# Kernel tuning notes

Hardware: AMD Instinct MI355X
Metric: run time of the kernel (lower is better)

## Reference

```python
import jax, jax.numpy as jnp
import numpy as np

B, S, C = 64, 1024, 512
EPS = 1e-5

def setup_inputs() -> dict:
    key = jax.random.key(0)
    k1, k2, k3 = jax.random.split(key, 3)
    x = jax.random.normal(k1, (B, S, C), dtype=jnp.float32)
    # LayerNorm affine over normalized_shape=[S, C]
    ln_w = jnp.ones((S, C), dtype=jnp.float32)
    ln_b = jnp.zeros((S, C), dtype=jnp.float32)
    # Linear(seq_len, seq_len): torch init U(-1/sqrt(S), 1/sqrt(S))
    bound = 1.0 / np.sqrt(S)
    lin_w = jax.random.uniform(k2, (S, S), jnp.float32, -bound, bound)
    lin_b = jax.random.uniform(k3, (S,), jnp.float32, -bound, bound)
    return {"x": x, "ln_w": ln_w, "ln_b": ln_b, "lin_w": lin_w, "lin_b": lin_b}

def reference(x, ln_w, ln_b, lin_w, lin_b):
    # LayerNorm over last two dims [S, C]
    mu = jnp.mean(x, axis=(1, 2), keepdims=True)
    var = jnp.mean(jnp.square(x - mu), axis=(1, 2), keepdims=True)
    h = (x - mu) * jax.lax.rsqrt(var + EPS) * ln_w + ln_b
    # permute -> [B, C, S], linear over S, relu, permute back, residual
    # fused as einsum over the seq axis directly (no explicit transpose)
    y = jnp.einsum('bsc,ts->btc', h, lin_w) + lin_b[None, :, None]
    y = jax.nn.relu(y)
    return x + y
```

## Files before the change

kernel.cpp:

```cpp
#include <hip/hip_runtime.h>
#include <stdint.h>

#define BB 64
#define SS 1024
#define CC 512
#define EPS 1e-5f

typedef __attribute__((ext_vector_type(8))) __bf16 bf16x8;
typedef __attribute__((ext_vector_type(8))) unsigned short ushort8v;
typedef __attribute__((ext_vector_type(4))) float f32x4;

__device__ __forceinline__ unsigned short f2bf(float f) {
    unsigned int u = __builtin_bit_cast(unsigned int, f);
    u += 0x7fffu + ((u >> 16) & 1u);
    return (unsigned short)(u >> 16);
}

__global__ __launch_bounds__(256) void k_convert_w(const float* __restrict__ w,
                                                   unsigned short* __restrict__ wb) {
    int i = blockIdx.x * 256 + threadIdx.x;
    float4 v = ((const float4*)w)[i];
    ushort4 o;
    o.x = f2bf(v.x); o.y = f2bf(v.y); o.z = f2bf(v.z); o.w = f2bf(v.w);
    ((ushort4*)wb)[i] = o;
}

__global__ __launch_bounds__(256) void k_stats1(const float* __restrict__ x,
                                                float* __restrict__ psum,
                                                float* __restrict__ psq) {
    int b = blockIdx.x >> 5, g = blockIdx.x & 31;
    const float4* x4 = (const float4*)(x + (size_t)b * SS * CC + (size_t)g * 16384);
    float s = 0.f, q = 0.f;
    int t = threadIdx.x;
#pragma unroll
    for (int i = 0; i < 16; ++i) {
        float4 v = x4[t + i * 256];
        s += v.x + v.y + v.z + v.w;
        q += v.x * v.x + v.y * v.y + v.z * v.z + v.w * v.w;
    }
    for (int off = 32; off; off >>= 1) {
        s += __shfl_down(s, off, 64);
        q += __shfl_down(q, off, 64);
    }
    __shared__ float ls[4], lq[4];
    int w = t >> 6;
    if ((t & 63) == 0) { ls[w] = s; lq[w] = q; }
    __syncthreads();
    if (t == 0) {
        psum[blockIdx.x] = ls[0] + ls[1] + ls[2] + ls[3];
        psq[blockIdx.x]  = lq[0] + lq[1] + lq[2] + lq[3];
    }
}

__global__ __launch_bounds__(64) void k_stats2(const float* __restrict__ psum,
                                               const float* __restrict__ psq,
                                               float* __restrict__ mu,
                                               float* __restrict__ rsig) {
    int b = blockIdx.x, t = threadIdx.x;
    float s = (t < 32) ? psum[b * 32 + t] : 0.f;
    float q = (t < 32) ? psq[b * 32 + t] : 0.f;
    for (int off = 32; off; off >>= 1) {
        s += __shfl_down(s, off, 64);
        q += __shfl_down(q, off, 64);
    }
    if (t == 0) {
        const float inv = 1.f / (float)(SS * CC);
        float m = s * inv;
        float v = q * inv - m * m;
        mu[b] = m;
        rsig[b] = rsqrtf(v + EPS);
    }
}

__global__ __launch_bounds__(256) void k_norm_t(const float* __restrict__ x,
                                                const float* __restrict__ lnw,
                                                const float* __restrict__ lnb,
                                                const float* __restrict__ muA,
                                                const float* __restrict__ rsA,
                                                unsigned short* __restrict__ Ht) {
    int idx = blockIdx.x;
    int b = idx >> 7;
    int rem = idx & 127;
    int s0 = (rem >> 3) << 6;
    int c0 = (rem & 7) << 6;
    float mu = muA[b], rs = rsA[b];
    __shared__ uint32_t lds[64 * 33];
    int t = threadIdx.x;
    int cq = t & 15, spA = t >> 4;
#pragma unroll
    for (int h = 0; h < 2; ++h) {
        int sp = spA + h * 16;
        int sl = s0 + 2 * sp;
        int cc = c0 + 4 * cq;
        size_t xb = ((size_t)b * SS + sl) * CC + cc;
        size_t lb = (size_t)sl * CC + cc;
        float4 xv0 = *(const float4*)(x + xb);
        float4 xv1 = *(const float4*)(x + xb + CC);
        float4 wv0 = *(const float4*)(lnw + lb);
        float4 wv1 = *(const float4*)(lnw + lb + CC);
        float4 bv0 = *(const float4*)(lnb + lb);
        float4 bv1 = *(const float4*)(lnb + lb + CC);
        uint32_t u0 = (uint32_t)f2bf((xv0.x - mu) * rs * wv0.x + bv0.x) |
                      ((uint32_t)f2bf((xv1.x - mu) * rs * wv1.x + bv1.x) << 16);
        uint32_t u1 = (uint32_t)f2bf((xv0.y - mu) * rs * wv0.y + bv0.y) |
                      ((uint32_t)f2bf((xv1.y - mu) * rs * wv1.y + bv1.y) << 16);
        uint32_t u2 = (uint32_t)f2bf((xv0.z - mu) * rs * wv0.z + bv0.z) |
                      ((uint32_t)f2bf((xv1.z - mu) * rs * wv1.z + bv1.z) << 16);
        uint32_t u3 = (uint32_t)f2bf((xv0.w - mu) * rs * wv0.w + bv0.w) |
                      ((uint32_t)f2bf((xv1.w - mu) * rs * wv1.w + bv1.w) << 16);
        lds[(4 * cq + 0) * 33 + sp] = u0;
        lds[(4 * cq + 1) * 33 + sp] = u1;
        lds[(4 * cq + 2) * 33 + sp] = u2;
        lds[(4 * cq + 3) * 33 + sp] = u3;
    }
    __syncthreads();
    int spq = t & 7, clA = t >> 3;
#pragma unroll
    for (int h = 0; h < 2; ++h) {
        int cl = clA + h * 32;
        uint4 v;
        v.x = lds[cl * 33 + spq * 4 + 0];
        v.y = lds[cl * 33 + spq * 4 + 1];
        v.z = lds[cl * 33 + spq * 4 + 2];
        v.w = lds[cl * 33 + spq * 4 + 3];
        size_t o = (((size_t)b * CC + c0 + cl) * SS + (size_t)s0 + spq * 8) >> 3;
        ((uint4*)Ht)[o] = v;
    }
}

__global__ __launch_bounds__(256) void k_gemm(const unsigned short* __restrict__ A,
                                              const unsigned short* __restrict__ Bt,
                                              const float* __restrict__ x,
                                              const float* __restrict__ linb,
                                              float* __restrict__ out) {
    const int b = blockIdx.z;
    const int tm = blockIdx.y;
    const int tn = blockIdx.x;
    __shared__ __align__(16) unsigned short As[128 * 32];
    __shared__ __align__(16) unsigned short Bs[128 * 32];
    const int tid = threadIdx.x;
    const int lane = tid & 63;
    const int w = tid >> 6;
    const int wm = w >> 1, wn = w & 1;
    const int quad = lane >> 4, l15 = lane & 15;

    f32x4 acc[4][4];
#pragma unroll
    for (int mi = 0; mi < 4; ++mi)
#pragma unroll
        for (int ni = 0; ni < 4; ++ni)
            acc[mi][ni] = (f32x4){0.f, 0.f, 0.f, 0.f};

    const unsigned short* Ab = A + (size_t)(tm * 128) * 1024;
    const unsigned short* Bb = Bt + ((size_t)b * 512 + tn * 128) * 1024;
    const int srow = tid >> 2;
    const int scol = (tid & 3) * 8;

    for (int k0 = 0; k0 < 1024; k0 += 32) {
        __syncthreads();
#pragma unroll
        for (int q = 0; q < 2; ++q) {
            const unsigned short* ga = Ab + (size_t)(q * 64 + srow) * 1024 + k0 + scol;
            const unsigned short* gb = Bb + (size_t)(q * 64 + srow) * 1024 + k0 + scol;
            __builtin_amdgcn_global_load_lds(
                (const __attribute__((address_space(1))) void*)ga,
                (__attribute__((address_space(3))) void*)(As + q * 2048 + w * 512),
                16, 0, 0);
            __builtin_amdgcn_global_load_lds(
                (const __attribute__((address_space(1))) void*)gb,
                (__attribute__((address_space(3))) void*)(Bs + q * 2048 + w * 512),
                16, 0, 0);
        }
        __syncthreads();

        bf16x8 av[4], bv[4];
#pragma unroll
        for (int i = 0; i < 4; ++i) {
            ushort8v a = *(const ushort8v*)&As[(wm * 64 + i * 16 + l15) * 32 + quad * 8];
            ushort8v bfr = *(const ushort8v*)&Bs[(wn * 64 + i * 16 + l15) * 32 + quad * 8];
            av[i] = __builtin_bit_cast(bf16x8, a);
            bv[i] = __builtin_bit_cast(bf16x8, bfr);
        }
#pragma unroll
        for (int mi = 0; mi < 4; ++mi)
#pragma unroll
            for (int ni = 0; ni < 4; ++ni)
                acc[mi][ni] = __builtin_amdgcn_mfma_f32_16x16x32_bf16(
                    av[mi], bv[ni], acc[mi][ni], 0, 0, 0);
    }

#pragma unroll
    for (int mi = 0; mi < 4; ++mi) {
#pragma unroll
        for (int r = 0; r < 4; ++r) {
            int tt = tm * 128 + wm * 64 + mi * 16 + quad * 4 + r;
            float lb = linb[tt];
#pragma unroll
            for (int ni = 0; ni < 4; ++ni) {
                int cc = tn * 128 + wn * 64 + ni * 16 + l15;
                size_t o = ((size_t)b * SS + tt) * CC + cc;
                float v = acc[mi][ni][r] + lb;
                v = v > 0.f ? v : 0.f;
                out[o] = x[o] + v;
            }
        }
    }
}

extern "C" void kernel_launch(void* const* d_in, const int* in_sizes, int n_in,
                              void* d_out, int out_size, void* d_ws, size_t ws_size,
                              hipStream_t stream) {
    (void)in_sizes; (void)n_in; (void)out_size; (void)ws_size;
    const float* x    = (const float*)d_in[0];
    const float* lnw  = (const float*)d_in[1];
    const float* lnb  = (const float*)d_in[2];
    const float* linw = (const float*)d_in[3];
    const float* linb = (const float*)d_in[4];
    float* out = (float*)d_out;

    char* ws = (char*)d_ws;
    unsigned short* Wb = (unsigned short*)ws;
    unsigned short* Ht = (unsigned short*)(ws + (2u << 20));
    float* psum = (float*)(ws + (66u << 20));
    float* psq  = psum + 2048;
    float* mu   = psq + 2048;
    float* rsig = mu + 64;

    k_convert_w<<<1024, 256, 0, stream>>>(linw, Wb);
    k_stats1<<<2048, 256, 0, stream>>>(x, psum, psq);
    k_stats2<<<64, 64, 0, stream>>>(psum, psq, mu, rsig);
    k_norm_t<<<8192, 256, 0, stream>>>(x, lnw, lnb, mu, rsig, Ht);
    dim3 g(4, 8, 64);
    k_gemm<<<g, 256, 0, stream>>>(Wb, Ht, x, linb, out);
}
```

Before: 386.1 us.

## Double-buffer GEMM LDS tiles and fold prep kernels into fewer launches

The GEMM now uses two LDS buffers per operand. It prefetches the next K-slice with global_load_lds while MFMAs run on the current one, which also removes one barrier per iteration. The LDS tile layout is reorganised so each wave loads and reads contiguous 16x32 blocks in MFMA lane order. On the prep side, the weight bf16 conversion is merged into the stats kernel as extra blocks, and the final mean/rsqrt reduction moves into the normalize kernel, cutting two launches. The cost is doubled LDS use, and every normalize block redundantly re-reduces the 32 partials.

Result: slower. 413.0 us (+7.0%).

```diff
diff --git a/kernel.cpp b/kernel.cpp
--- a/kernel.cpp
+++ b/kernel.cpp
@@ -16,22 +16,23 @@
     return (unsigned short)(u >> 16);
 }
 
-__global__ __launch_bounds__(256) void k_convert_w(const float* __restrict__ w,
-                                                   unsigned short* __restrict__ wb) {
-    int i = blockIdx.x * 256 + threadIdx.x;
-    float4 v = ((const float4*)w)[i];
-    ushort4 o;
-    o.x = f2bf(v.x); o.y = f2bf(v.y); o.z = f2bf(v.z); o.w = f2bf(v.w);
-    ((ushort4*)wb)[i] = o;
-}
-
-__global__ __launch_bounds__(256) void k_stats1(const float* __restrict__ x,
-                                                float* __restrict__ psum,
-                                                float* __restrict__ psq) {
+__global__ __launch_bounds__(256) void k_prep(const float* __restrict__ x,
+                                              const float* __restrict__ w,
+                                              float* __restrict__ psum,
+                                              float* __restrict__ psq,
+                                              unsigned short* __restrict__ wb) {
+    int t = threadIdx.x;
+    if (blockIdx.x >= 2048) {
+        int i = (blockIdx.x - 2048) * 256 + t;
+        float4 v = ((const float4*)w)[i];
+        ushort4 o;
+        o.x = f2bf(v.x); o.y = f2bf(v.y); o.z = f2bf(v.z); o.w = f2bf(v.w);
+        ((ushort4*)wb)[i] = o;
+        return;
+    }
     int b = blockIdx.x >> 5, g = blockIdx.x & 31;
     const float4* x4 = (const float4*)(x + (size_t)b * SS * CC + (size_t)g * 16384);
     float s = 0.f, q = 0.f;
-    int t = threadIdx.x;
 #pragma unroll
     for (int i = 0; i < 16; ++i) {
         float4 v = x4[t + i * 256];
@@ -43,8 +44,8 @@
         q += __shfl_down(q, off, 64);
     }
     __shared__ float ls[4], lq[4];
-    int w = t >> 6;
-    if ((t & 63) == 0) { ls[w] = s; lq[w] = q; }
+    int wv = t >> 6;
+    if ((t & 63) == 0) { ls[wv] = s; lq[wv] = q; }
     __syncthreads();
     if (t == 0) {
         psum[blockIdx.x] = ls[0] + ls[1] + ls[2] + ls[3];
@@ -52,40 +53,39 @@
     }
 }
 
-__global__ __launch_bounds__(64) void k_stats2(const float* __restrict__ psum,
-                                               const float* __restrict__ psq,
-                                               float* __restrict__ mu,
-                                               float* __restrict__ rsig) {
-    int b = blockIdx.x, t = threadIdx.x;
-    float s = (t < 32) ? psum[b * 32 + t] : 0.f;
-    float q = (t < 32) ? psq[b * 32 + t] : 0.f;
-    for (int off = 32; off; off >>= 1) {
-        s += __shfl_down(s, off, 64);
-        q += __shfl_down(q, off, 64);
-    }
-    if (t == 0) {
-        const float inv = 1.f / (float)(SS * CC);
-        float m = s * inv;
-        float v = q * inv - m * m;
-        mu[b] = m;
-        rsig[b] = rsqrtf(v + EPS);
-    }
-}
-
 __global__ __launch_bounds__(256) void k_norm_t(const float* __restrict__ x,
                                                 const float* __restrict__ lnw,
                                                 const float* __restrict__ lnb,
-                                                const float* __restrict__ muA,
-                                                const float* __restrict__ rsA,
+                                                const float* __restrict__ psum,
+                                                const float* __restrict__ psq,
                                                 unsigned short* __restrict__ Ht) {
     int idx = blockIdx.x;
     int b = idx >> 7;
     int rem = idx & 127;
     int s0 = (rem >> 3) << 6;
     int c0 = (rem & 7) << 6;
-    float mu = muA[b], rs = rsA[b];
+    int t = threadIdx.x;
+
+    __shared__ float s_stats[2];
+    if (t < 64) {
+        float s = (t < 32) ? psum[b * 32 + t] : 0.f;
+        float q = (t < 32) ? psq[b * 32 + t] : 0.f;
+        for (int off = 16; off; off >>= 1) {
+            s += __shfl_down(s, off, 64);
+            q += __shfl_down(q, off, 64);
+        }
+        if (t == 0) {
+            const float inv = 1.f / (float)(SS * CC);
+            float m = s * inv;
+            float v = q * inv - m * m;
+            s_stats[0] = m;
+            s_stats[1] = rsqrtf(v + EPS);
+        }
+    }
+    __syncthreads();
+    float mu = s_stats[0], rs = s_stats[1];
+
     __shared__ uint32_t lds[64 * 33];
-    int t = threadIdx.x;
     int cq = t & 15, spA = t >> 4;
 #pragma unroll
     for (int h = 0; h < 2; ++h) {
@@ -136,8 +136,8 @@
     const int b = blockIdx.z;
     const int tm = blockIdx.y;
     const int tn = blockIdx.x;
-    __shared__ __align__(16) unsigned short As[128 * 32];
-    __shared__ __align__(16) unsigned short Bs[128 * 32];
+    __shared__ __align__(16) unsigned short As[2][4096];
+    __shared__ __align__(16) unsigned short Bs[2][4096];
     const int tid = threadIdx.x;
     const int lane = tid & 63;
     const int w = tid >> 6;
@@ -151,35 +151,42 @@
         for (int ni = 0; ni < 4; ++ni)
             acc[mi][ni] = (f32x4){0.f, 0.f, 0.f, 0.f};
 
-    const unsigned short* Ab = A + (size_t)(tm * 128) * 1024;
-    const unsigned short* Bb = Bt + ((size_t)b * 512 + tn * 128) * 1024;
-    const int srow = tid >> 2;
-    const int scol = (tid & 3) * 8;
-
-    for (int k0 = 0; k0 < 1024; k0 += 32) {
+    const unsigned short* gA = A + ((size_t)(tm * 128 + w * 16 + l15)) * 1024 + quad * 8;
+    const unsigned short* gB = Bt + ((size_t)b * 512 + tn * 128 + w * 16 + l15) * 1024 + quad * 8;
+
+#pragma unroll
+    for (int q = 0; q < 2; ++q) {
+        __builtin_amdgcn_global_load_lds(
+            (const __attribute__((address_space(1))) void*)(gA + q * 65536),
+            (__attribute__((address_space(3))) void*)(As[0] + (q * 4 + w) * 512), 16, 0, 0);
+        __builtin_amdgcn_global_load_lds(
+            (const __attribute__((address_space(1))) void*)(gB + q * 65536),
+            (__attribute__((address_space(3))) void*)(Bs[0] + (q * 4 + w) * 512), 16, 0, 0);
+    }
+
+    for (int it = 0; it < 32; ++it) {
         __syncthreads();
-#pragma unroll
-        for (int q = 0; q < 2; ++q) {
-            const unsigned short* ga = Ab + (size_t)(q * 64 + srow) * 1024 + k0 + scol;
-            const unsigned short* gb = Bb + (size_t)(q * 64 + srow) * 1024 + k0 + scol;
-            __builtin_amdgcn_global_load_lds(
-                (const __attribute__((address_space(1))) void*)ga,
-                (__attribute__((address_space(3))) void*)(As + q * 2048 + w * 512),
-                16, 0, 0);
-            __builtin_amdgcn_global_load_lds(
-                (const __attribute__((address_space(1))) void*)gb,
-                (__attribute__((address_space(3))) void*)(Bs + q * 2048 + w * 512),
-                16, 0, 0);
-        }
-        __syncthreads();
-
+        if (it < 31) {
+            const int k0 = (it + 1) * 32;
+            const int nb = (it + 1) & 1;
+#pragma unroll
+            for (int q = 0; q < 2; ++q) {
+                __builtin_amdgcn_global_load_lds(
+                    (const __attribute__((address_space(1))) void*)(gA + q * 65536 + k0),
+                    (__attribute__((address_space(3))) void*)(As[nb] + (q * 4 + w) * 512), 16, 0, 0);
+                __builtin_amdgcn_global_load_lds(
+                    (const __attribute__((address_space(1))) void*)(gB + q * 65536 + k0),
+                    (__attribute__((address_space(3))) void*)(Bs[nb] + (q * 4 + w) * 512), 16, 0, 0);
+            }
+        }
+        const int cb = it & 1;
         bf16x8 av[4], bv[4];
 #pragma unroll
         for (int i = 0; i < 4; ++i) {
-            ushort8v a = *(const ushort8v*)&As[(wm * 64 + i * 16 + l15) * 32 + quad * 8];
-            ushort8v bfr = *(const ushort8v*)&Bs[(wn * 64 + i * 16 + l15) * 32 + quad * 8];
+            ushort8v a = *(const ushort8v*)(As[cb] + (wm * 4 + i) * 512 + lane * 8);
+            ushort8v bb = *(const ushort8v*)(Bs[cb] + (wn * 4 + i) * 512 + lane * 8);
             av[i] = __builtin_bit_cast(bf16x8, a);
-            bv[i] = __builtin_bit_cast(bf16x8, bfr);
+            bv[i] = __builtin_bit_cast(bf16x8, bb);
         }
 #pragma unroll
         for (int mi = 0; mi < 4; ++mi)
@@ -223,13 +230,9 @@
     unsigned short* Ht = (unsigned short*)(ws + (2u << 20));
     float* psum = (float*)(ws + (66u << 20));
     float* psq  = psum + 2048;
-    float* mu   = psq + 2048;
-    float* rsig = mu + 64;
-
-    k_convert_w<<<1024, 256, 0, stream>>>(linw, Wb);
-    k_stats1<<<2048, 256, 0, stream>>>(x, psum, psq);
-    k_stats2<<<64, 64, 0, stream>>>(psum, psq, mu, rsig);
-    k_norm_t<<<8192, 256, 0, stream>>>(x, lnw, lnb, mu, rsig, Ht);
+
+    k_prep<<<3072, 256, 0, stream>>>(x, linw, psum, psq, Wb);
+    k_norm_t<<<8192, 256, 0, stream>>>(x, lnw, lnb, psum, psq, Ht);
     dim3 g(4, 8, 64);
     k_gemm<<<g, 256, 0, stream>>>(Wb, Ht, x, linb, out);
 }
```
